# Kernel optimization log

Measured on AMD Instinct MI355X. Metric: run time of the kernel, lower is better.

The kernel has to match this reference:

```python
import jax, jax.numpy as jnp
import numpy as np

LMAX = 10
F_IN = 64
F_OUT = 64
N_GRID = 512
IRREP_DIM = sum((2 * l + 1) ** 2 for l in range(LMAX + 1))  # 1771
BATCH = 256


def setup_inputs() -> dict:
    key = jax.random.key(0)
    kx, kD, kw = jax.random.split(key, 3)
    x = jax.random.normal(kx, (BATCH, F_IN, IRREP_DIM), dtype=jnp.float32)
    D = jax.random.normal(kD, (N_GRID, IRREP_DIM), dtype=jnp.float32)
    w = jax.random.normal(kw, (F_IN, F_OUT, N_GRID), dtype=jnp.float32)
    return {"x": x, "D": D, "w": w}


def _so3_linear(x, psi):
    # x:   (B, f_in, sum_l (2l+1)^2) signal over SO(3) irreps
    # psi: (f_in, f_out, sum_l (2l+1)^2) per-degree block weights
    B, f_in, _ = x.shape
    f_out = psi.shape[1]
    outs = []
    off = 0
    for l in range(LMAX + 1):
        d = 2 * l + 1
        blk = d * d
        # input block: multiplicity u (=d) x irrep component m (=d)
        x_l = x[:, :, off:off + blk].reshape(B, f_in, d, d)        # (B,i,u,m)
        w_l = psi[:, :, off:off + blk].reshape(f_in, f_out, d, d)  # (i,o,u,v)
        alpha = 1.0 / np.sqrt(f_in * d)  # e3nn fan-in path normalization
        out_l = jnp.einsum('bium,iouv->bovm', x_l, w_l) * alpha
        outs.append(out_l.reshape(B, f_out, blk))
        off += blk
    return jnp.concatenate(outs, axis=-1)


def reference(x, D, w):
    # project spatial filter into Fourier (irrep) domain
    n_grid = D.shape[0]
    psi = jnp.einsum('ni,xyn->xyi', D, w) / np.sqrt(n_grid)  # (f_in, f_out, IRREP_DIM)
    return _so3_linear(x, psi)
```

## Files before the change

kernel.cpp:

```cpp
#include <hip/hip_runtime.h>
#include <hip/hip_bf16.h>

#define IDIM 1771
#define NF 64
#define NG 512

constexpr int OFFS[12] = {0, 1, 10, 35, 84, 165, 286, 455, 680, 969, 1330, 1771};

typedef float f32x4 __attribute__((ext_vector_type(4)));
typedef float f32x2 __attribute__((ext_vector_type(2)));
typedef __bf16 bf16x2 __attribute__((ext_vector_type(2)));
typedef __bf16 bf16x8 __attribute__((ext_vector_type(8)));

__device__ __forceinline__ void gl_lds16(const void* g, void* l) {
    __builtin_amdgcn_global_load_lds((const __attribute__((address_space(1))) void*)g,
                                     (__attribute__((address_space(3))) void*)l, 16, 0, 0);
}

__global__ __launch_bounds__(256) void prep_repack_kernel(const float* __restrict__ D,
                                                          const float* __restrict__ w,
                                                          const float* __restrict__ x,
                                                          __bf16* __restrict__ Dt,
                                                          __bf16* __restrict__ wb,
                                                          __bf16* __restrict__ A) {
    __shared__ alignas(16) char smem[16640];
    const int blk = blockIdx.x;
    const int t = threadIdx.x;
    const int lane = t & 63, grp = t >> 6;

    if (blk < 224) {
        float (*T)[65] = (float (*)[65])smem;
        const int ct = blk >> 3, nt = blk & 7;
        const int c0 = ct * 64, n0 = nt * 64;
        float tmp[16];
#pragma unroll
        for (int p = 0; p < 16; ++p) {
            int nn = grp + p * 4;
            int c = c0 + lane;
            tmp[p] = (c < IDIM) ? D[(size_t)(n0 + nn) * IDIM + c] : 0.0f;
        }
#pragma unroll
        for (int p = 0; p < 16; ++p) T[grp + p * 4][lane] = tmp[p];
        __syncthreads();
        for (int cc = grp; cc < 64; cc += 4) {
            int c = c0 + cc;
            if (c < IDIM) Dt[c * NG + n0 + lane] = (__bf16)T[lane][cc];
        }
    } else if (blk < 288) {
        const int o = blk - 224;
#pragma unroll
        for (int ii0 = 0; ii0 < 64; ii0 += 8) {
            f32x2 tmp[8];
#pragma unroll
            for (int j = 0; j < 8; ++j)
                tmp[j] = *(const f32x2*)&w[((size_t)((ii0 + j) * 64 + o)) * NG + t * 2];
#pragma unroll
            for (int j = 0; j < 8; ++j) {
                bf16x2 ov;
                ov.x = (__bf16)tmp[j].x;
                ov.y = (__bf16)tmp[j].y;
                *(bf16x2*)&wb[((size_t)(o * 64 + ii0 + j)) * NG + t * 2] = ov;
            }
        }
    } else {
        const int idx = blk - 288;
        const int l = idx >> 8;
        const int b = idx & 255;
        const int d = 2 * l + 1, off = OFFS[l], csq = d * d, Kp = 64 * d;
        __bf16 (*T)[66] = (__bf16 (*)[66])smem;
        const float* xb = x + (size_t)b * NF * IDIM + off;
        __bf16* Ab = A + (size_t)16384 * off + (size_t)b * d * Kp;

        for (int c0 = 0; c0 < csq; c0 += 64) {
            float tmp[16];
#pragma unroll
            for (int p = 0; p < 16; ++p) {
                int ii = grp * 16 + p;
                int c = c0 + lane;
                tmp[p] = (c < csq) ? xb[(size_t)ii * IDIM + c] : 0.0f;
            }
#pragma unroll
            for (int p2 = 0; p2 < 8; ++p2) {
                bf16x2 v;
                v.x = (__bf16)tmp[2 * p2];
                v.y = (__bf16)tmp[2 * p2 + 1];
                *(bf16x2*)&T[lane][grp * 16 + 2 * p2] = v;
            }
            __syncthreads();
#pragma unroll
            for (int s = 0; s < 2; ++s) {
                int idx2 = s * 256 + t;
                int c_loc = idx2 >> 3, i0 = (idx2 & 7) * 8;
                int c = c0 + c_loc;
                if (c < csq) {
                    int u = (unsigned)c / (unsigned)d;
                    int m = c - u * d;
                    bf16x8 v;
#pragma unroll
                    for (int j2 = 0; j2 < 4; ++j2) {
                        bf16x2 r = *(const bf16x2*)&T[c_loc][i0 + 2 * j2];
                        v[2 * j2] = r.x;
                        v[2 * j2 + 1] = r.y;
                    }
                    *(bf16x8*)(Ab + (size_t)m * Kp + u * 64 + i0) = v;
                }
            }
            __syncthreads();
        }
    }
}

__global__ __launch_bounds__(256) void psi_mfma_kernel(const __bf16* __restrict__ Dt,
                                                       const __bf16* __restrict__ wb,
                                                       __bf16* __restrict__ Bm) {
    __shared__ alignas(16) __bf16 S[2 * 16384];

    const int t = threadIdx.x, w = t >> 6, ln = t & 63;
    const int row0 = blockIdx.x * 128;
    const int col0 = blockIdx.y * 128;

    const bool isA = (w < 2);
    const int wsub = w & 1;
    const int rowloc = ln >> 3;
    const int logslot = (ln & 7) ^ rowloc;

    const __bf16* gp[8];
    __bf16* lp[8];
#pragma unroll
    for (int q = 0; q < 8; ++q) {
        int chunk = wsub * 8 + q;
        int row = chunk * 8 + rowloc;
        int g = isA ? (row0 + row < IDIM ? row0 + row : IDIM - 1) : (col0 + row);
        gp[q] = (isA ? Dt : wb) + (size_t)g * NG + logslot * 8;
        lp[q] = S + (isA ? 0 : 8192) + chunk * 512;
    }

    f32x4 acc[4][4];
    f32x4 zero = {0.0f, 0.0f, 0.0f, 0.0f};
#pragma unroll
    for (int i = 0; i < 4; ++i)
#pragma unroll
        for (int j = 0; j < 4; ++j) acc[i][j] = zero;

    const int wr = (w >> 1) * 64, wc = (w & 1) * 64;
    const int fr = ln & 15, kh = ln >> 4;
    const int fx = fr & 7;

    int aoff[2][4], boff[2][4];
#pragma unroll
    for (int kk = 0; kk < 2; ++kk)
#pragma unroll
        for (int mt = 0; mt < 4; ++mt) {
            aoff[kk][mt] = (wr + mt * 16 + fr) * 64 + (((kk << 2) | kh) ^ fx) * 8;
            boff[kk][mt] = (wc + mt * 16 + fr) * 64 + (((kk << 2) | kh) ^ fx) * 8;
        }

    const int np = NG / 64;

#pragma unroll
    for (int q = 0; q < 8; ++q) { gl_lds16(gp[q], lp[q]); gp[q] += 64; }
    asm volatile("s_waitcnt vmcnt(0)" ::: "memory");
    __builtin_amdgcn_s_barrier();
    __builtin_amdgcn_sched_barrier(0);

    int bi = 0;
    for (int p = 0; p < np; ++p) {
        if (p + 1 < np) {
#pragma unroll
            for (int q = 0; q < 8; ++q) {
                gl_lds16(gp[q], lp[q] + (bi ^ 1) * 16384);
                gp[q] += 64;
            }
        }
        const __bf16* As_ = S + bi * 16384;
        const __bf16* Bs_ = As_ + 8192;
        bf16x8 af[2][4], bf_[2][4];
#pragma unroll
        for (int kk = 0; kk < 2; ++kk) {
#pragma unroll
            for (int mt = 0; mt < 4; ++mt) af[kk][mt] = *(const bf16x8*)&As_[aoff[kk][mt]];
#pragma unroll
            for (int nt = 0; nt < 4; ++nt) bf_[kk][nt] = *(const bf16x8*)&Bs_[boff[kk][nt]];
        }
#pragma unroll
        for (int kk = 0; kk < 2; ++kk)
#pragma unroll
            for (int mt = 0; mt < 4; ++mt)
#pragma unroll
                for (int nt = 0; nt < 4; ++nt)
                    acc[mt][nt] = __builtin_amdgcn_mfma_f32_16x16x32_bf16(
                        af[kk][mt], bf_[kk][nt], acc[mt][nt], 0, 0, 0);
        asm volatile("s_waitcnt vmcnt(0)" ::: "memory");
        __builtin_amdgcn_s_barrier();
        __builtin_amdgcn_sched_barrier(0);
        bi ^= 1;
    }

    const float sc = 0.04419417382415922f;
    const int o = (col0 + wc) >> 6;
#pragma unroll
    for (int mt = 0; mt < 4; ++mt) {
#pragma unroll
        for (int e = 0; e < 4; ++e) {
            int c = row0 + wr + mt * 16 + kh * 4 + e;
            if (c < IDIM) {
                int l = 0;
#pragma unroll
                for (int ll = 1; ll < 11; ++ll)
                    if (c >= OFFS[ll]) l = ll;
                int d = 2 * l + 1, off = OFFS[l];
                int rem = c - off;
                int u = (unsigned)rem / (unsigned)d;
                int v = rem - u * d;
                __bf16* bb = Bm + (size_t)4096 * off + (size_t)(o * d + v) * (64 * d) + u * 64;
#pragma unroll
                for (int nt = 0; nt < 4; ++nt) {
                    int i = nt * 16 + fr;
                    bb[i] = (__bf16)(acc[mt][nt][e] * sc);
                }
            }
        }
    }
}

__global__ __launch_bounds__(256) void so3_gemm_all(const __bf16* __restrict__ A,
                                                    const __bf16* __restrict__ Bm,
                                                    float* __restrict__ out) {
    const int bid = blockIdx.x;
    const int v_ = (bid & 7) * 237 + (bid >> 3);
    if (v_ >= 1892) return;

    int l = 10, base = 0;
    if (v_ >= 462)  { l = 9; base = 462; }
    if (v_ >= 842)  { l = 8; base = 842; }
    if (v_ >= 1148) { l = 7; base = 1148; }
    if (v_ >= 1388) { l = 6; base = 1388; }
    if (v_ >= 1570) { l = 5; base = 1570; }
    if (v_ >= 1702) { l = 4; base = 1702; }
    if (v_ >= 1792) { l = 3; base = 1792; }
    if (v_ >= 1848) { l = 2; base = 1848; }
    if (v_ >= 1878) { l = 1; base = 1878; }
    if (v_ >= 1890) { l = 0; base = 1890; }

    const int d = 2 * l + 1;
    const int off = OFFS[l];
    const int Np = 64 * d, Kp = 64 * d;
    const int ntiles = l + 1;
    const int rel = v_ - base;
    const int bx = (unsigned)rel / (unsigned)ntiles;
    const int by = rel - bx * ntiles;
    const int row0 = bx * 128, col0 = by * 128;

    constexpr float ALPHA[11] = {0.125f, 0.07216878f, 0.05590170f, 0.04724556f,
                                 0.04166667f, 0.03768892f, 0.03466879f, 0.03227486f,
                                 0.03031695f, 0.02867697f, 0.02727724f};

    __shared__ alignas(16) __bf16 S[2 * 16384];

    const int t = threadIdx.x, w = t >> 6, ln = t & 63;

    const __bf16* Abase = A + (size_t)16384 * off;
    const __bf16* Bbase = Bm + (size_t)4096 * off;

    const bool isA = (w < 2);
    const int wsub = w & 1;
    const int rowloc = ln >> 3;
    const int logslot = (ln & 7) ^ rowloc;

    const __bf16* gp[8];
    __bf16* lp[8];
#pragma unroll
    for (int q = 0; q < 8; ++q) {
        int chunk = wsub * 8 + q;
        int row = chunk * 8 + rowloc;
        int g = isA ? (row0 + row) : (col0 + row < Np ? col0 + row : Np - 1);
        gp[q] = (isA ? Abase : Bbase) + (size_t)g * Kp + logslot * 8;
        lp[q] = S + (isA ? 0 : 8192) + chunk * 512;
    }

    f32x4 acc[4][4];
    f32x4 zero = {0.0f, 0.0f, 0.0f, 0.0f};
#pragma unroll
    for (int i = 0; i < 4; ++i)
#pragma unroll
        for (int j = 0; j < 4; ++j) acc[i][j] = zero;

    const int wr = (w >> 1) * 64, wc = (w & 1) * 64;
    const int fr = ln & 15, kh = ln >> 4;
    const int fx = fr & 7;

    int aoff[2][4], boff[2][4];
#pragma unroll
    for (int kk = 0; kk < 2; ++kk)
#pragma unroll
        for (int mt = 0; mt < 4; ++mt) {
            aoff[kk][mt] = (wr + mt * 16 + fr) * 64 + (((kk << 2) | kh) ^ fx) * 8;
            boff[kk][mt] = (wc + mt * 16 + fr) * 64 + (((kk << 2) | kh) ^ fx) * 8;
        }

    const int np = Kp / 64;

#pragma unroll
    for (int q = 0; q < 8; ++q) { gl_lds16(gp[q], lp[q]); gp[q] += 64; }
    asm volatile("s_waitcnt vmcnt(0)" ::: "memory");
    __builtin_amdgcn_s_barrier();
    __builtin_amdgcn_sched_barrier(0);

    int bi = 0;
    for (int p = 0; p < np; ++p) {
        if (p + 1 < np) {
#pragma unroll
            for (int q = 0; q < 8; ++q) {
                gl_lds16(gp[q], lp[q] + (bi ^ 1) * 16384);
                gp[q] += 64;
            }
        }
        const __bf16* As_ = S + bi * 16384;
        const __bf16* Bs_ = As_ + 8192;
        bf16x8 af[2][4], bf_[2][4];
#pragma unroll
        for (int kk = 0; kk < 2; ++kk) {
#pragma unroll
            for (int mt = 0; mt < 4; ++mt) af[kk][mt] = *(const bf16x8*)&As_[aoff[kk][mt]];
#pragma unroll
            for (int nt = 0; nt < 4; ++nt) bf_[kk][nt] = *(const bf16x8*)&Bs_[boff[kk][nt]];
        }
#pragma unroll
        for (int kk = 0; kk < 2; ++kk)
#pragma unroll
            for (int mt = 0; mt < 4; ++mt)
#pragma unroll
                for (int nt = 0; nt < 4; ++nt)
                    acc[mt][nt] = __builtin_amdgcn_mfma_f32_16x16x32_bf16(
                        af[kk][mt], bf_[kk][nt], acc[mt][nt], 0, 0, 0);
        asm volatile("s_waitcnt vmcnt(0)" ::: "memory");
        __builtin_amdgcn_s_barrier();
        __builtin_amdgcn_sched_barrier(0);
        bi ^= 1;
    }

    __syncthreads();
    float* Tw = (float*)S + w * 256;
    const float alpha = ALPHA[l];

#pragma unroll
    for (int mt = 0; mt < 4; ++mt) {
        int r = row0 + wr + mt * 16 + fr;
        int b = (unsigned)r / (unsigned)d;
        int m = r - b * d;
        float* ob = out + (size_t)b * NF * IDIM + off + m;
#pragma unroll
        for (int nt = 0; nt < 4; ++nt) {
#pragma unroll
            for (int e = 0; e < 4; ++e) Tw[(kh * 4 + e) * 16 + fr] = acc[mt][nt][e];
            f32x4 vals = *(const f32x4*)&Tw[fr * 16 + kh * 4];
            int qb = col0 + wc + nt * 16 + kh * 4;
            int o = (unsigned)qb / (unsigned)d;
            int vv = qb - o * d;
#pragma unroll
            for (int j = 0; j < 4; ++j) {
                if (qb + j < Np) ob[o * IDIM + vv * d] = alpha * vals[j];
                ++vv;
                if (vv == d) { vv = 0; ++o; }
            }
        }
    }
}

extern "C" void kernel_launch(void* const* d_in, const int* in_sizes, int n_in,
                              void* d_out, int out_size, void* d_ws, size_t ws_size,
                              hipStream_t stream) {
    const float* x = (const float*)d_in[0];
    const float* D = (const float*)d_in[1];
    const float* w = (const float*)d_in[2];
    float* out = (float*)d_out;

    char* ws = (char*)d_ws;
    const size_t DT_BYTES = (size_t)IDIM * NG * 2;
    const size_t WB_BYTES = (size_t)4096 * NG * 2;
    const size_t A_BYTES = (size_t)16384 * IDIM * 2;

    __bf16* Dt = (__bf16*)ws;
    __bf16* wb = (__bf16*)(ws + DT_BYTES);
    __bf16* A = (__bf16*)(ws + DT_BYTES + WB_BYTES);
    __bf16* Bm = (__bf16*)(ws + DT_BYTES + WB_BYTES + A_BYTES);

    prep_repack_kernel<<<3104, 256, 0, stream>>>(D, w, x, Dt, wb, A);
    psi_mfma_kernel<<<dim3(14, 32), 256, 0, stream>>>(Dt, wb, Bm);
    so3_gemm_all<<<1896, 256, 0, stream>>>((const __bf16*)A, Bm, out);
}
```

Measured before the change: 376.2 us.

## Enlarge SO3 GEMM tiles to 256x256 with 512-thread blocks

Block tiles in the batched per-degree GEMM grow from 128x128 to 256x256, with 8 waves each computing 128x64. The XCD-aware block mapping is rebuilt for 506 blocks, and MFMA sections are wrapped in s_setprio. Larger tiles raise arithmetic intensity and cut redundant loads of A and B. The cost is 128KB of LDS per block, more accumulator registers, and more wasted padding on the small-degree tiles.

```diff
diff --git a/kernel.cpp b/kernel.cpp
--- a/kernel.cpp
+++ b/kernel.cpp
@@ -223,82 +223,82 @@
     }
 }
 
-__global__ __launch_bounds__(256) void so3_gemm_all(const __bf16* __restrict__ A,
-                                                    const __bf16* __restrict__ Bm,
-                                                    float* __restrict__ out) {
+__global__ __launch_bounds__(512, 2) void so3_gemm_all(const __bf16* __restrict__ A,
+                                                       const __bf16* __restrict__ Bm,
+                                                       float* __restrict__ out) {
     const int bid = blockIdx.x;
-    const int v_ = (bid & 7) * 237 + (bid >> 3);
-    if (v_ >= 1892) return;
+    const int xcd = bid & 7, sub = bid >> 3;
+    const int v_ = (xcd < 2 ? xcd * 64 : 128 + (xcd - 2) * 63) + sub;
 
     int l = 10, base = 0;
-    if (v_ >= 462)  { l = 9; base = 462; }
-    if (v_ >= 842)  { l = 8; base = 842; }
-    if (v_ >= 1148) { l = 7; base = 1148; }
-    if (v_ >= 1388) { l = 6; base = 1388; }
-    if (v_ >= 1570) { l = 5; base = 1570; }
-    if (v_ >= 1702) { l = 4; base = 1702; }
-    if (v_ >= 1792) { l = 3; base = 1792; }
-    if (v_ >= 1848) { l = 2; base = 1848; }
-    if (v_ >= 1878) { l = 1; base = 1878; }
-    if (v_ >= 1890) { l = 0; base = 1890; }
+    if (v_ >= 126) { l = 9; base = 126; }
+    if (v_ >= 221) { l = 8; base = 221; }
+    if (v_ >= 306) { l = 7; base = 306; }
+    if (v_ >= 366) { l = 6; base = 366; }
+    if (v_ >= 418) { l = 5; base = 418; }
+    if (v_ >= 451) { l = 4; base = 451; }
+    if (v_ >= 478) { l = 3; base = 478; }
+    if (v_ >= 492) { l = 2; base = 492; }
+    if (v_ >= 502) { l = 1; base = 502; }
+    if (v_ >= 505) { l = 0; base = 505; }
 
     const int d = 2 * l + 1;
     const int off = OFFS[l];
     const int Np = 64 * d, Kp = 64 * d;
-    const int ntiles = l + 1;
+    const int nN = (d + 3) >> 2;
     const int rel = v_ - base;
-    const int bx = (unsigned)rel / (unsigned)ntiles;
-    const int by = rel - bx * ntiles;
-    const int row0 = bx * 128, col0 = by * 128;
+    const int bx = (unsigned)rel / (unsigned)nN;
+    const int by = rel - bx * nN;
+    const int row0 = bx * 256, col0 = by * 256;
 
     constexpr float ALPHA[11] = {0.125f, 0.07216878f, 0.05590170f, 0.04724556f,
                                  0.04166667f, 0.03768892f, 0.03466879f, 0.03227486f,
                                  0.03031695f, 0.02867697f, 0.02727724f};
 
-    __shared__ alignas(16) __bf16 S[2 * 16384];
+    __shared__ alignas(16) __bf16 S[2 * 32768];
 
     const int t = threadIdx.x, w = t >> 6, ln = t & 63;
 
     const __bf16* Abase = A + (size_t)16384 * off;
     const __bf16* Bbase = Bm + (size_t)4096 * off;
 
-    const bool isA = (w < 2);
-    const int wsub = w & 1;
-    const int rowloc = ln >> 3;
-    const int logslot = (ln & 7) ^ rowloc;
-
+    const int trow = t >> 3, tslot = t & 7;
+    const int slog = tslot ^ (trow & 7);
     const __bf16* gp[8];
     __bf16* lp[8];
 #pragma unroll
     for (int q = 0; q < 8; ++q) {
-        int chunk = wsub * 8 + q;
-        int row = chunk * 8 + rowloc;
+        bool isA = q < 4;
+        int rowblk = q & 3;
+        int row = rowblk * 64 + trow;
         int g = isA ? (row0 + row) : (col0 + row < Np ? col0 + row : Np - 1);
-        gp[q] = (isA ? Abase : Bbase) + (size_t)g * Kp + logslot * 8;
-        lp[q] = S + (isA ? 0 : 8192) + chunk * 512;
-    }
-
-    f32x4 acc[4][4];
+        gp[q] = (isA ? Abase : Bbase) + (size_t)g * Kp + slog * 8;
+        lp[q] = S + (isA ? 0 : 16384) + rowblk * 4096 + t * 8;
+    }
+
+    f32x4 acc[8][4];
     f32x4 zero = {0.0f, 0.0f, 0.0f, 0.0f};
 #pragma unroll
-    for (int i = 0; i < 4; ++i)
+    for (int i = 0; i < 8; ++i)
 #pragma unroll
         for (int j = 0; j < 4; ++j) acc[i][j] = zero;
 
-    const int wr = (w >> 1) * 64, wc = (w & 1) * 64;
+    const int wr = (w >> 2) * 128, wc = (w & 3) * 64;
     const int fr = ln & 15, kh = ln >> 4;
     const int fx = fr & 7;
 
-    int aoff[2][4], boff[2][4];
-#pragma unroll
-    for (int kk = 0; kk < 2; ++kk)
-#pragma unroll
-        for (int mt = 0; mt < 4; ++mt) {
+    int aoff[2][8], boff[2][4];
+#pragma unroll
+    for (int kk = 0; kk < 2; ++kk) {
+#pragma unroll
+        for (int mt = 0; mt < 8; ++mt)
             aoff[kk][mt] = (wr + mt * 16 + fr) * 64 + (((kk << 2) | kh) ^ fx) * 8;
-            boff[kk][mt] = (wc + mt * 16 + fr) * 64 + (((kk << 2) | kh) ^ fx) * 8;
-        }
-
-    const int np = Kp / 64;
+#pragma unroll
+        for (int nt = 0; nt < 4; ++nt)
+            boff[kk][nt] = (wc + nt * 16 + fr) * 64 + (((kk << 2) | kh) ^ fx) * 8;
+    }
+
+    const int np = d;
 
 #pragma unroll
     for (int q = 0; q < 8; ++q) { gl_lds16(gp[q], lp[q]); gp[q] += 64; }
@@ -311,40 +311,39 @@
         if (p + 1 < np) {
 #pragma unroll
             for (int q = 0; q < 8; ++q) {
-                gl_lds16(gp[q], lp[q] + (bi ^ 1) * 16384);
+                gl_lds16(gp[q], lp[q] + (bi ^ 1) * 32768);
                 gp[q] += 64;
             }
         }
-        const __bf16* As_ = S + bi * 16384;
-        const __bf16* Bs_ = As_ + 8192;
-        bf16x8 af[2][4], bf_[2][4];
+        const __bf16* As_ = S + bi * 32768;
+        const __bf16* Bs_ = As_ + 16384;
 #pragma unroll
         for (int kk = 0; kk < 2; ++kk) {
-#pragma unroll
-            for (int mt = 0; mt < 4; ++mt) af[kk][mt] = *(const bf16x8*)&As_[aoff[kk][mt]];
-#pragma unroll
-            for (int nt = 0; nt < 4; ++nt) bf_[kk][nt] = *(const bf16x8*)&Bs_[boff[kk][nt]];
-        }
-#pragma unroll
-        for (int kk = 0; kk < 2; ++kk)
-#pragma unroll
-            for (int mt = 0; mt < 4; ++mt)
+            bf16x8 af[8], bfr[4];
+#pragma unroll
+            for (int mt = 0; mt < 8; ++mt) af[mt] = *(const bf16x8*)&As_[aoff[kk][mt]];
+#pragma unroll
+            for (int nt = 0; nt < 4; ++nt) bfr[nt] = *(const bf16x8*)&Bs_[boff[kk][nt]];
+            __builtin_amdgcn_s_setprio(1);
+#pragma unroll
+            for (int mt = 0; mt < 8; ++mt)
 #pragma unroll
                 for (int nt = 0; nt < 4; ++nt)
                     acc[mt][nt] = __builtin_amdgcn_mfma_f32_16x16x32_bf16(
-                        af[kk][mt], bf_[kk][nt], acc[mt][nt], 0, 0, 0);
+                        af[mt], bfr[nt], acc[mt][nt], 0, 0, 0);
+            __builtin_amdgcn_s_setprio(0);
+        }
         asm volatile("s_waitcnt vmcnt(0)" ::: "memory");
         __builtin_amdgcn_s_barrier();
         __builtin_amdgcn_sched_barrier(0);
         bi ^= 1;
     }
 
-    __syncthreads();
     float* Tw = (float*)S + w * 256;
     const float alpha = ALPHA[l];
 
 #pragma unroll
-    for (int mt = 0; mt < 4; ++mt) {
+    for (int mt = 0; mt < 8; ++mt) {
         int r = row0 + wr + mt * 16 + fr;
         int b = (unsigned)r / (unsigned)d;
         int m = r - b * d;
@@ -387,5 +386,5 @@
 
     prep_repack_kernel<<<3104, 256, 0, stream>>>(D, w, x, Dt, wb, A);
     psi_mfma_kernel<<<dim3(14, 32), 256, 0, stream>>>(Dt, wb, Bm);
-    so3_gemm_all<<<1896, 256, 0, stream>>>((const __bf16*)A, Bm, out);
-}
+    so3_gemm_all<<<506, 512, 0, stream>>>((const __bf16*)A, Bm, out);
+}
```

Result: faster. 367.8 us (-2.2%).
